# Optimization experiments

Hardware: AMD Instinct MI355X
Metric: run time of the kernel (lower is better)

## Reference

```python
import jax, jax.numpy as jnp
import numpy as np

B, S, S2, NH, H, NKEYS = 2, 4096, 2048, 8, 64, 64


def setup_inputs() -> dict:
    key = jax.random.key(0)
    kq, kk, kv, ki = jax.random.split(key, 4)
    q = jax.random.normal(kq, (B, S2, NH, H), dtype=jnp.float32)
    k = jax.random.normal(kk, (B, S, NH, H), dtype=jnp.float32)
    v = jax.random.normal(kv, (B, S, NH, H), dtype=jnp.float32)
    indices_select = jax.random.randint(ki, (B, S2, NKEYS), 0, S, dtype=jnp.int64)
    return {"q": q, "k": k, "v": v, "indices_select": indices_select}


def reference(q, k, v, indices_select):
    b, s, nh, h = k.shape
    q = q * (h ** -0.5)
    # gather n random keys/values per (batch, query): (b, s2, n, nh, h)
    batch_idx = jnp.arange(b)[:, None, None]
    k_g = k[batch_idx, indices_select]
    v_g = v[batch_idx, indices_select]
    # scores over the n gathered keys, per head: (b, q, k, n)
    A = jnp.einsum('bqnh,bqknh->bqkn', q, k_g)
    A = jax.nn.softmax(A, axis=-2)  # softmax over gathered-key dim (torch dim=-2)
    z = jnp.einsum('bqkn,bqknh->bqnh', A, v_g)
    return z
```

## Files before the change

kernel.cpp:

```cpp
#include <hip/hip_runtime.h>


#define BB 2
#define SS 4096
#define S2V 2048
#define NHV 8
#define HV 64
#define NKV 64

__global__ __launch_bounds__(256, 4)
void rsa_kernel(const float* __restrict__ q, const float* __restrict__ k,
                const float* __restrict__ v, const int* __restrict__ idx,
                float* __restrict__ out) {
    const int lane = threadIdx.x & 63;
    const int w    = threadIdx.x >> 6;
    const int bi   = blockIdx.x;

    const int combo = bi & 15;
    const int b     = combo >> 3;
    const int n     = combo & 7;
    const int qi    = ((bi >> 4) << 2) + w;

    const int g  = lane >> 4;
    const int hc = lane & 15;

    const size_t bq = (size_t)b * S2V + qi;

    const float* qrow = q + (bq * NHV + n) * HV;
    const float4 qv = *(const float4*)(qrow + hc * 4);
    const float4 q4 = make_float4(qv.x * 0.125f, qv.y * 0.125f,
                                  qv.z * 0.125f, qv.w * 0.125f);

    const int my_off = idx[bq * NKV + lane] * (NHV * HV);

    int offs[16];
#pragma unroll
    for (int it = 0; it < 16; ++it)
        offs[it] = __shfl(my_off, it * 4 + g, 64);

    const float* kb = k + ((size_t)b * SS * NHV + n) * HV;
    const float* vb = v + ((size_t)b * SS * NHV + n) * HV;

    float sc[16];
#pragma unroll
    for (int it = 0; it < 16; ++it) {
        const float4 k4 = *(const float4*)(kb + offs[it] + hc * 4);
        float d = k4.x * q4.x + k4.y * q4.y + k4.z * q4.z + k4.w * q4.w;
        d += __shfl_xor(d, 1);
        d += __shfl_xor(d, 2);
        d += __shfl_xor(d, 4);
        d += __shfl_xor(d, 8);
        sc[it] = d;
    }

    float m = sc[0];
#pragma unroll
    for (int it = 1; it < 16; ++it) m = fmaxf(m, sc[it]);
    m = fmaxf(m, __shfl_xor(m, 16));
    m = fmaxf(m, __shfl_xor(m, 32));

    float ssum = 0.f;
#pragma unroll
    for (int it = 0; it < 16; ++it) {
        sc[it] = __expf(sc[it] - m);
        ssum += sc[it];
    }
    ssum += __shfl_xor(ssum, 16);
    ssum += __shfl_xor(ssum, 32);
    const float rs = __frcp_rn(ssum);

    float4 z = make_float4(0.f, 0.f, 0.f, 0.f);
#pragma unroll
    for (int it = 0; it < 16; ++it) {
        const float4 v4 = *(const float4*)(vb + offs[it] + hc * 4);
        const float p = sc[it];
        z.x = fmaf(p, v4.x, z.x);
        z.y = fmaf(p, v4.y, z.y);
        z.z = fmaf(p, v4.z, z.z);
        z.w = fmaf(p, v4.w, z.w);
    }
    z.x += __shfl_xor(z.x, 16); z.y += __shfl_xor(z.y, 16);
    z.z += __shfl_xor(z.z, 16); z.w += __shfl_xor(z.w, 16);
    z.x += __shfl_xor(z.x, 32); z.y += __shfl_xor(z.y, 32);
    z.z += __shfl_xor(z.z, 32); z.w += __shfl_xor(z.w, 32);

    if (g == 0) {
        float4 zo = make_float4(z.x * rs, z.y * rs, z.z * rs, z.w * rs);
        *(float4*)(out + (bq * NHV + n) * HV + hc * 4) = zo;
    }
}

extern "C" void kernel_launch(void* const* d_in, const int* in_sizes, int n_in,
                              void* d_out, int out_size, void* d_ws, size_t ws_size,
                              hipStream_t stream) {
    const float* q   = (const float*)d_in[0];
    const float* k   = (const float*)d_in[1];
    const float* v   = (const float*)d_in[2];
    const int*   idx = (const int*)d_in[3];
    float*       out = (float*)d_out;

    const int n_units = BB * S2V * NHV;
    const int blocks  = n_units / 4;
    rsa_kernel<<<blocks, 256, 0, stream>>>(q, k, v, idx, out);
}
```

Baseline: 125.4 us.

## Stage gathered K/V rows into LDS via async global_load_lds

K and V rows gathered by the index list are now copied straight into shared memory with the async global-to-LDS load builtin, instead of being loaded into registers. The V loads are issued before the softmax runs, so that work can overlap with the outstanding memory requests. Blocks shrink to two waves with 32KB of LDS each. This frees vector registers but limits how many waves fit on a CU, which may hurt latency hiding for this gather-bound kernel.

```diff
diff --git a/kernel.cpp b/kernel.cpp
--- a/kernel.cpp
+++ b/kernel.cpp
@@ -1,4 +1,5 @@
 #include <hip/hip_runtime.h>
+#include <stdint.h>
 
 
 #define BB 2
@@ -8,7 +9,14 @@
 #define HV 64
 #define NKV 64
 
-__global__ __launch_bounds__(256, 4)
+__device__ __forceinline__ void async16(const float* g, float* l) {
+    __builtin_amdgcn_global_load_lds(
+        (const __attribute__((address_space(1))) void*)g,
+        (__attribute__((address_space(3))) void*)l,
+        16, 0, 0);
+}
+
+__global__ __launch_bounds__(128)
 void rsa_kernel(const float* __restrict__ q, const float* __restrict__ k,
                 const float* __restrict__ v, const int* __restrict__ idx,
                 float* __restrict__ out) {
@@ -19,10 +27,13 @@
     const int combo = bi & 15;
     const int b     = combo >> 3;
     const int n     = combo & 7;
-    const int qi    = ((bi >> 4) << 2) + w;
+    const int qi    = ((bi >> 4) << 1) + w;
 
     const int g  = lane >> 4;
     const int hc = lane & 15;
+
+    __shared__ float buf[2][4096];
+    float* mybuf = &buf[w][0];
 
     const size_t bq = (size_t)b * S2V + qi;
 
@@ -33,24 +44,33 @@
 
     const int my_off = idx[bq * NKV + lane] * (NHV * HV);
 
-    int offs[16];
-#pragma unroll
-    for (int it = 0; it < 16; ++it)
-        offs[it] = __shfl(my_off, it * 4 + g, 64);
-
     const float* kb = k + ((size_t)b * SS * NHV + n) * HV;
     const float* vb = v + ((size_t)b * SS * NHV + n) * HV;
+
+#pragma unroll
+    for (int it = 0; it < 16; ++it) {
+        const int off = __shfl(my_off, it * 4 + g, 64);
+        async16(kb + off + hc * 4, mybuf + it * 256);
+    }
+    __syncthreads();
 
     float sc[16];
 #pragma unroll
     for (int it = 0; it < 16; ++it) {
-        const float4 k4 = *(const float4*)(kb + offs[it] + hc * 4);
+        const float4 k4 = *(const float4*)(mybuf + it * 256 + lane * 4);
         float d = k4.x * q4.x + k4.y * q4.y + k4.z * q4.z + k4.w * q4.w;
         d += __shfl_xor(d, 1);
         d += __shfl_xor(d, 2);
         d += __shfl_xor(d, 4);
         d += __shfl_xor(d, 8);
         sc[it] = d;
+    }
+    __syncthreads();
+
+#pragma unroll
+    for (int it = 0; it < 16; ++it) {
+        const int off = __shfl(my_off, it * 4 + g, 64);
+        async16(vb + off + hc * 4, mybuf + it * 256);
     }
 
     float m = sc[0];
@@ -69,10 +89,12 @@
     ssum += __shfl_xor(ssum, 32);
     const float rs = __frcp_rn(ssum);
 
+    __syncthreads();
+
     float4 z = make_float4(0.f, 0.f, 0.f, 0.f);
 #pragma unroll
     for (int it = 0; it < 16; ++it) {
-        const float4 v4 = *(const float4*)(vb + offs[it] + hc * 4);
+        const float4 v4 = *(const float4*)(mybuf + it * 256 + lane * 4);
         const float p = sc[it];
         z.x = fmaf(p, v4.x, z.x);
         z.y = fmaf(p, v4.y, z.y);
@@ -100,6 +122,6 @@
     float*       out = (float*)d_out;
 
     const int n_units = BB * S2V * NHV;
-    const int blocks  = n_units / 4;
-    rsa_kernel<<<blocks, 256, 0, stream>>>(q, k, v, idx, out);
+    const int blocks  = n_units / 2;
+    rsa_kernel<<<blocks, 128, 0, stream>>>(q, k, v, idx, out);
 }
```

After: 154.7 us. 23.4% more time.
